# Performance work log

Measured on AMD Instinct MI355X. Metric: run time of the kernel, lower is better.

## Reference

```python
import jax, jax.numpy as jnp
import numpy as np

E = 1024
H = 16
DH = E // H
HID = E // 4  # sync_gate hidden


def setup_inputs() -> dict:
    key = jax.random.key(0)
    ks = jax.random.split(key, 16)
    s = lambda k, shp, fan_in: jax.random.normal(k, shp, dtype=jnp.float32) / np.sqrt(fan_in)
    return {
        "x": jax.random.normal(ks[0], (2, 2048, E), dtype=jnp.float32),
        "sync_features": jax.random.normal(ks[1], (2, E), dtype=jnp.float32),
        "Wq": s(ks[2], (E, E), E), "bq": jnp.zeros((E,), jnp.float32),
        "Wk": s(ks[3], (E, E), E), "bk": jnp.zeros((E,), jnp.float32),
        "Wv": s(ks[4], (E, E), E), "bv": jnp.zeros((E,), jnp.float32),
        "Ws1": s(ks[5], (E, HID), E), "bs1": jnp.zeros((HID,), jnp.float32),
        "Ws2": s(ks[6], (HID, H), HID), "bs2": jnp.zeros((H,), jnp.float32),
        "Wo": s(ks[7], (E, E), E), "bo": jnp.zeros((E,), jnp.float32),
    }


def reference(x, sync_features, Wq, bq, Wk, bk, Wv, bv, Ws1, bs1, Ws2, bs2, Wo, bo):
    B, S, _ = x.shape
    # QKV projections, split into heads: [B,S,H,DH]
    q = (x @ Wq + bq).reshape(B, S, H, DH)
    k = (x @ Wk + bk).reshape(B, S, H, DH)
    v = (x @ Wv + bv).reshape(B, S, H, DH)
    # scores: [B,H,S,S]
    scores = jnp.einsum('bihd,bjhd->bhij', q, k) / np.sqrt(DH).astype(np.float32)
    # per-head sync gate: [B,H] -> broadcast multiply BEFORE softmax
    sw = jax.nn.sigmoid(jax.nn.relu(sync_features @ Ws1 + bs1) @ Ws2 + bs2)
    scores = scores * sw[:, :, None, None]
    attn = jax.nn.softmax(scores, axis=-1)
    # dropout is identity in eval mode
    ctx = jnp.einsum('bhij,bjhd->bihd', attn, v).reshape(B, S, E)
    out = ctx @ Wo + bo
    return out, attn.mean(axis=1)
```

## Files before the change

### kernel.cpp

```cpp
#include <hip/hip_runtime.h>

#define B_ 2
#define S_ 2048
#define E_ 1024
#define H_ 16
#define DH_ 64
#define HID_ 256
#define M_ (B_*S_)

typedef __attribute__((ext_vector_type(8))) short s16x8;
typedef __attribute__((ext_vector_type(4))) float f32x4;
typedef unsigned int u32;
typedef unsigned short u16;
typedef u32 __attribute__((address_space(1))) gu32;
typedef u32 __attribute__((address_space(3))) lu32;

#define MFMA_B16(a,b,c) __builtin_amdgcn_mfma_f32_16x16x32_bf16((a),(b),(c),0,0,0)

__device__ __forceinline__ f32x4 fzero() { f32x4 z = {0.f, 0.f, 0.f, 0.f}; return z; }

__device__ __forceinline__ u16 f2bf(float x) {
    u32 u = __float_as_uint(x);
    u32 r = u + 0x7FFFu + ((u >> 16) & 1u);
    return (u16)(r >> 16);
}
__device__ __forceinline__ float bf2f(u16 b) {
    return __uint_as_float(((u32)b) << 16);
}
__device__ __forceinline__ void gload16(const void* gsrc, void* ldst) {
    __builtin_amdgcn_global_load_lds((const gu32*)gsrc, (lu32*)ldst, 16, 0, 0);
}
__device__ __forceinline__ s16x8 lds_frag(const u16* base, int byt) {
    return *(const s16x8*)((const char*)base + byt);
}

__global__ __launch_bounds__(256)
void zfill(float* __restrict__ out, int n)
{
    const int i = blockIdx.x * 256 + threadIdx.x;
    if (i < n) out[i] = 0.f;
}

__global__ __launch_bounds__(256)
void gate_kernel(const float* __restrict__ sync_f,
                 const float* __restrict__ Ws1, const float* __restrict__ bs1,
                 const float* __restrict__ Ws2, const float* __restrict__ bs2,
                 float* __restrict__ sw)
{
    __shared__ float xs[E_];
    __shared__ float hid[HID_];
    const int b = blockIdx.x, t = threadIdx.x;
    for (int i = t; i < E_; i += 256) xs[i] = sync_f[b * E_ + i];
    __syncthreads();
    float acc = bs1[t];
    for (int k = 0; k < E_; ++k) acc = fmaf(xs[k], Ws1[k * HID_ + t], acc);
    hid[t] = fmaxf(acc, 0.f);
    __syncthreads();
    if (t < H_) {
        float a = bs2[t];
        for (int k = 0; k < HID_; ++k) a = fmaf(hid[k], Ws2[k * H_ + t], a);
        sw[b * H_ + t] = 1.f / (1.f + __expf(-a));
    }
}

__global__ __launch_bounds__(256)
void split_x(const float* __restrict__ X, u16* __restrict__ Xhi, u16* __restrict__ Xlo)
{
    const int i = blockIdx.x * 256 + threadIdx.x;
    if (i >= M_ * E_ / 8) return;
    const float4 a = ((const float4*)X)[2 * i];
    const float4 bq = ((const float4*)X)[2 * i + 1];
    float v[8] = {a.x, a.y, a.z, a.w, bq.x, bq.y, bq.z, bq.w};
    s16x8 h, l;
#pragma unroll
    for (int e = 0; e < 8; ++e) {
        u16 hb = f2bf(v[e]);
        h[e] = (short)hb;
        l[e] = (short)f2bf(v[e] - bf2f(hb));
    }
    ((s16x8*)Xhi)[i] = h;
    ((s16x8*)Xlo)[i] = l;
}

__global__ __launch_bounds__(256)
void split_tw(const float* __restrict__ W, u16* __restrict__ Thi, u16* __restrict__ Tlo)
{
    __shared__ float t[64][65];
    const int k0 = blockIdx.y * 64;
    const int n0 = blockIdx.x * 64;
    const int tid = threadIdx.x;
    const int rr = tid >> 4;
    const int cc = (tid & 15) * 4;
#pragma unroll
    for (int p = 0; p < 4; ++p) {
        float4 v = *(const float4*)&W[(size_t)(k0 + p * 16 + rr) * E_ + n0 + cc];
        t[p * 16 + rr][cc + 0] = v.x;
        t[p * 16 + rr][cc + 1] = v.y;
        t[p * 16 + rr][cc + 2] = v.z;
        t[p * 16 + rr][cc + 3] = v.w;
    }
    __syncthreads();
    const int on = tid >> 2;
    const int ok = (tid & 3) * 16;
    s16x8 h0, h1, l0, l1;
#pragma unroll
    for (int j = 0; j < 8; ++j) {
        float v = t[ok + j][on];
        u16 hb = f2bf(v);
        h0[j] = (short)hb; l0[j] = (short)f2bf(v - bf2f(hb));
        float v2 = t[ok + 8 + j][on];
        u16 hb2 = f2bf(v2);
        h1[j] = (short)hb2; l1[j] = (short)f2bf(v2 - bf2f(hb2));
    }
    size_t o = (size_t)(n0 + on) * E_ + k0 + ok;
    *(s16x8*)&Thi[o] = h0;  *(s16x8*)&Thi[o + 8] = h1;
    *(s16x8*)&Tlo[o] = l0;  *(s16x8*)&Tlo[o + 8] = l1;
}

template<int MODE>
__global__ __launch_bounds__(256)
void gemm_mfma(const u16* __restrict__ Ahi, const u16* __restrict__ Alo,
               const u16* __restrict__ Bhi, const u16* __restrict__ Blo,
               const float* __restrict__ bias,
               float* __restrict__ OutF, u16* __restrict__ OutHi, u16* __restrict__ OutLo)
{
    __shared__ u16 lA[2][128 * 32];
    __shared__ u16 lB[2][128 * 32];
    const int m0 = blockIdx.y * 128, n0 = blockIdx.x * 128;
    const int tid = threadIdx.x;
    const int w = tid >> 6, l = tid & 63;
    const int l15 = l & 15, l4 = l >> 4;
    const int wm = w >> 1, wn = w & 1;

    f32x4 acc[4][4];
#pragma unroll
    for (int i = 0; i < 4; ++i)
#pragma unroll
        for (int j = 0; j < 4; ++j) acc[i][j] = fzero();

    for (int k0 = 0; k0 < E_; k0 += 32) {
        __syncthreads();
#pragma unroll
        for (int jj = 0; jj < 8; ++jj) {
            const int idx = w * 8 + jj, tt = idx >> 3, q = idx & 7;
            const int r = q * 16 + (l >> 2);
            const int s = l & 3;
            const int g = s ^ ((r >> 1) & 3);
            const u16* src;
            if (tt == 0)      src = Ahi + (size_t)(m0 + r) * E_ + k0 + 8 * g;
            else if (tt == 1) src = Alo + (size_t)(m0 + r) * E_ + k0 + 8 * g;
            else if (tt == 2) src = Bhi + (size_t)(n0 + r) * E_ + k0 + 8 * g;
            else              src = Blo + (size_t)(n0 + r) * E_ + k0 + 8 * g;
            u16* base = (tt < 2) ? lA[tt] : lB[tt - 2];
            gload16(src, (char*)base + q * 1024);
        }
        __syncthreads();

        s16x8 af[2][4];
#pragma unroll
        for (int hl = 0; hl < 2; ++hl)
#pragma unroll
            for (int mf = 0; mf < 4; ++mf) {
                const int row = wm * 64 + mf * 16 + l15;
                af[hl][mf] = lds_frag(lA[hl], row * 64 + ((l4 ^ ((row >> 1) & 3)) << 4));
            }
#pragma unroll
        for (int nf = 0; nf < 4; ++nf) {
            const int rowb = wn * 64 + nf * 16 + l15;
            const int byt = rowb * 64 + ((l4 ^ ((rowb >> 1) & 3)) << 4);
            s16x8 b0 = lds_frag(lB[0], byt);
            s16x8 b1 = lds_frag(lB[1], byt);
#pragma unroll
            for (int mf = 0; mf < 4; ++mf) {
                acc[mf][nf] = MFMA_B16(af[0][mf], b0, acc[mf][nf]);
                acc[mf][nf] = MFMA_B16(af[0][mf], b1, acc[mf][nf]);
                acc[mf][nf] = MFMA_B16(af[1][mf], b0, acc[mf][nf]);
            }
        }
    }

#pragma unroll
    for (int mf = 0; mf < 4; ++mf)
#pragma unroll
        for (int nf = 0; nf < 4; ++nf) {
            const int n = n0 + wn * 64 + nf * 16 + l15;
            const float bb = bias[n];
#pragma unroll
            for (int rr = 0; rr < 4; ++rr) {
                const int m = m0 + wm * 64 + mf * 16 + l4 * 4 + rr;
                const float v = acc[mf][nf][rr] + bb;
                if (MODE == 0) {
                    OutF[(size_t)m * E_ + n] = v;
                } else {
                    const int bat = m >> 11, s = m & (S_ - 1);
                    const int hh = n >> 6, dh = n & 63;
                    const size_t o = (MODE == 1)
                        ? (((size_t)(bat * H_ + hh) * S_ + s) * DH_ + dh)
                        : (((size_t)(bat * H_ + hh) * DH_ + dh) * S_ + s);
                    const u16 hb = f2bf(v);
                    OutHi[o] = hb;
                    OutLo[o] = f2bf(v - bf2f(hb));
                }
            }
        }
}

__global__ __launch_bounds__(256)
void attn_pass1(const u16* __restrict__ qhi, const u16* __restrict__ qlo,
                const u16* __restrict__ khi, const u16* __restrict__ klo,
                const u16* __restrict__ vthi, const u16* __restrict__ vtlo,
                const float* __restrict__ sw,
                u16* __restrict__ ctxhi, u16* __restrict__ ctxlo,
                float* __restrict__ invl)
{
    __shared__ u16 lK[2][64 * 64];
    __shared__ u16 lV[2][64 * 64];
    __shared__ float lP[128 * 64];
    const int b = blockIdx.z, h = blockIdx.y, i0 = blockIdx.x * 128;
    const int tid = threadIdx.x;
    const int w = tid >> 6, l = tid & 63;
    const int l15 = l & 15, l4 = l >> 4;
    const size_t bh = (size_t)(b * H_ + h);
    const float scl = sw[b * H_ + h] * 0.125f;

    s16x8 qf[2][2][2];
#pragma unroll
    for (int hl = 0; hl < 2; ++hl)
#pragma unroll
        for (int rf = 0; rf < 2; ++rf)
#pragma unroll
            for (int kc = 0; kc < 2; ++kc) {
                const int row = i0 + w * 32 + rf * 16 + l15;
                const u16* src = (hl ? qlo : qhi) + (bh * S_ + row) * DH_ + kc * 32 + 8 * l4;
                qf[hl][rf][kc] = *(const s16x8*)src;
            }

    f32x4 cacc[2][4];
    float l_acc[2][4];
#pragma unroll
    for (int rf = 0; rf < 2; ++rf) {
#pragma unroll
        for (int df = 0; df < 4; ++df) cacc[rf][df] = fzero();
#pragma unroll
        for (int rr = 0; rr < 4; ++rr) l_acc[rf][rr] = 0.f;
    }

    for (int j0 = 0; j0 < S_; j0 += 64) {
        __syncthreads();
#pragma unroll
        for (int jj = 0; jj < 8; ++jj) {
            const int idx = w * 8 + jj, tt = idx >> 3, q = idx & 7;
            const int r = q * 8 + (l >> 3);
            const int s = l & 7;
            const int g = s ^ (r & 7);
            const u16* src;
            if (tt == 0)      src = khi  + (bh * S_ + j0 + r) * DH_ + 8 * g;
            else if (tt == 1) src = klo  + (bh * S_ + j0 + r) * DH_ + 8 * g;
            else if (tt == 2) src = vthi + (bh * DH_ + r) * S_ + j0 + 8 * g;
            else              src = vtlo + (bh * DH_ + r) * S_ + j0 + 8 * g;
            u16* base = (tt < 2) ? lK[tt] : lV[tt - 2];
            gload16(src, (char*)base + q * 1024);
        }
        __syncthreads();

        f32x4 p[2][4];
#pragma unroll
        for (int rf = 0; rf < 2; ++rf)
#pragma unroll
            for (int nf = 0; nf < 4; ++nf) p[rf][nf] = fzero();
#pragma unroll
        for (int kc = 0; kc < 2; ++kc) {
            s16x8 kb[2][4];
#pragma unroll
            for (int hl = 0; hl < 2; ++hl)
#pragma unroll
                for (int nf = 0; nf < 4; ++nf) {
                    const int j = nf * 16 + l15;
                    kb[hl][nf] = lds_frag(lK[hl], j * 128 + (((kc * 4 + l4) ^ (j & 7)) << 4));
                }
#pragma unroll
            for (int rf = 0; rf < 2; ++rf)
#pragma unroll
                for (int nf = 0; nf < 4; ++nf) {
                    p[rf][nf] = MFMA_B16(qf[0][rf][kc], kb[0][nf], p[rf][nf]);
                    p[rf][nf] = MFMA_B16(qf[0][rf][kc], kb[1][nf], p[rf][nf]);
                    p[rf][nf] = MFMA_B16(qf[1][rf][kc], kb[0][nf], p[rf][nf]);
                }
        }
#pragma unroll
        for (int rf = 0; rf < 2; ++rf)
#pragma unroll
            for (int nf = 0; nf < 4; ++nf) {
                const int jcol = nf * 16 + l15;
#pragma unroll
                for (int rr = 0; rr < 4; ++rr) {
                    const float e = __expf(p[rf][nf][rr] * scl);
                    l_acc[rf][rr] += e;
                    const int irow = w * 32 + rf * 16 + l4 * 4 + rr;
                    const int byt = irow * 256 +
                        ((((jcol >> 2) ^ ((irow >> 1) & 7)) << 4) | ((jcol & 3) << 2));
                    *(float*)((char*)lP + byt) = e;
                }
            }
#pragma unroll
        for (int kc = 0; kc < 2; ++kc) {
            s16x8 vb[2][4];
#pragma unroll
            for (int hl = 0; hl < 2; ++hl)
#pragma unroll
                for (int df = 0; df < 4; ++df) {
                    const int d = df * 16 + l15;
                    vb[hl][df] = lds_frag(lV[hl], d * 128 + (((kc * 4 + l4) ^ (d & 7)) << 4));
                }
#pragma unroll
            for (int rf = 0; rf < 2; ++rf) {
                const int irow = w * 32 + rf * 16 + l15;
                const int msk = (irow >> 1) & 7;
                float pv8[8];
#pragma unroll
                for (int hh = 0; hh < 2; ++hh) {
                    const int slot = kc * 8 + 2 * l4 + hh;
                    const f32x4 t4 = *(const f32x4*)((const char*)lP +
                                        irow * 256 + ((slot ^ msk) << 4));
                    pv8[hh * 4 + 0] = t4[0]; pv8[hh * 4 + 1] = t4[1];
                    pv8[hh * 4 + 2] = t4[2]; pv8[hh * 4 + 3] = t4[3];
                }
                s16x8 ph, pl;
#pragma unroll
                for (int e = 0; e < 8; ++e) {
                    const u16 hb = f2bf(pv8[e]);
                    ph[e] = (short)hb;
                    pl[e] = (short)f2bf(pv8[e] - bf2f(hb));
                }
#pragma unroll
                for (int df = 0; df < 4; ++df) {
                    cacc[rf][df] = MFMA_B16(ph, vb[0][df], cacc[rf][df]);
                    cacc[rf][df] = MFMA_B16(ph, vb[1][df], cacc[rf][df]);
                    cacc[rf][df] = MFMA_B16(pl, vb[0][df], cacc[rf][df]);
                }
            }
        }
    }

#pragma unroll
    for (int rf = 0; rf < 2; ++rf)
#pragma unroll
        for (int rr = 0; rr < 4; ++rr) {
#pragma unroll
            for (int off = 1; off < 16; off <<= 1)
                l_acc[rf][rr] += __shfl_xor(l_acc[rf][rr], off);
        }
#pragma unroll
    for (int rf = 0; rf < 2; ++rf)
#pragma unroll
        for (int rr = 0; rr < 4; ++rr) {
            const float inv = 1.f / l_acc[rf][rr];
            const int srow = i0 + w * 32 + rf * 16 + l4 * 4 + rr;
            if (l15 == 0) invl[bh * S_ + srow] = inv;
#pragma unroll
            for (int df = 0; df < 4; ++df) {
                const float v = cacc[rf][df][rr] * inv;
                const size_t o = ((size_t)b * S_ + srow) * E_ + h * DH_ + df * 16 + l15;
                const u16 hb = f2bf(v);
                ctxhi[o] = hb;
                ctxlo[o] = f2bf(v - bf2f(hb));
            }
        }
}

__global__ __launch_bounds__(256)
void attn_mean(const u16* __restrict__ qhi, const u16* __restrict__ qlo,
               const u16* __restrict__ khi, const u16* __restrict__ klo,
               const float* __restrict__ sw, const float* __restrict__ invl,
               float* __restrict__ amean)
{
    __shared__ u16 lQ[2][128 * 64];
    __shared__ u16 lKm[2][128 * 64];
    const int b = blockIdx.z, i0 = blockIdx.y * 128, j0 = blockIdx.x * 128;
    const int tid = threadIdx.x;
    const int w = tid >> 6, l = tid & 63;
    const int l15 = l & 15, l4 = l >> 4;

    f32x4 acc[2][8];
#pragma unroll
    for (int rf = 0; rf < 2; ++rf)
#pragma unroll
        for (int nf = 0; nf < 8; ++nf) acc[rf][nf] = fzero();

    for (int h = 0; h < H_; ++h) {
        const size_t bh = (size_t)(b * H_ + h);
        __syncthreads();
#pragma unroll
        for (int jj = 0; jj < 16; ++jj) {
            const int idx = w * 16 + jj, tt = idx >> 4, q = idx & 15;
            const int r = q * 8 + (l >> 3);
            const int s = l & 7;
            const int g = s ^ (r & 7);
            const u16* bsrc = (tt == 0) ? qhi : (tt == 1) ? qlo : (tt == 2) ? khi : klo;
            const int row0 = (tt < 2) ? i0 : j0;
            const u16* src = bsrc + (bh * S_ + row0 + r) * DH_ + 8 * g;
            u16* base = (tt == 0) ? lQ[0] : (tt == 1) ? lQ[1]
                      : (tt == 2) ? lKm[0] : lKm[1];
            gload16(src, (char*)base + q * 1024);
        }
        __syncthreads();

        const float scl = sw[b * H_ + h] * 0.125f;
        float ivl[2][4];
#pragma unroll
        for (int rf = 0; rf < 2; ++rf)
#pragma unroll
            for (int rr = 0; rr < 4; ++rr)
                ivl[rf][rr] = invl[bh * S_ + i0 + w * 32 + rf * 16 + l4 * 4 + rr];

        f32x4 sc[2][8];
#pragma unroll
        for (int rf = 0; rf < 2; ++rf)
#pragma unroll
            for (int nf = 0; nf < 8; ++nf) sc[rf][nf] = fzero();
#pragma unroll
        for (int kc = 0; kc < 2; ++kc) {
            s16x8 qa[2][2];
#pragma unroll
            for (int hl = 0; hl < 2; ++hl)
#pragma unroll
                for (int rf = 0; rf < 2; ++rf) {
                    const int row = w * 32 + rf * 16 + l15;
                    qa[hl][rf] = lds_frag(lQ[hl],
                        row * 128 + (((kc * 4 + l4) ^ (row & 7)) << 4));
                }
#pragma unroll
            for (int nf = 0; nf < 8; ++nf) {
                const int j = nf * 16 + l15;
                const int byt = j * 128 + (((kc * 4 + l4) ^ (j & 7)) << 4);
                const s16x8 kb0 = lds_frag(lKm[0], byt);
                const s16x8 kb1 = lds_frag(lKm[1], byt);
#pragma unroll
                for (int rf = 0; rf < 2; ++rf) {
                    sc[rf][nf] = MFMA_B16(qa[0][rf], kb0, sc[rf][nf]);
                    sc[rf][nf] = MFMA_B16(qa[0][rf], kb1, sc[rf][nf]);
                    sc[rf][nf] = MFMA_B16(qa[1][rf], kb0, sc[rf][nf]);
                }
            }
        }
#pragma unroll
        for (int rf = 0; rf < 2; ++rf)
#pragma unroll
            for (int nf = 0; nf < 8; ++nf)
#pragma unroll
                for (int rr = 0; rr < 4; ++rr)
                    acc[rf][nf][rr] = fmaf(__expf(sc[rf][nf][rr] * scl), ivl[rf][rr],
                                           acc[rf][nf][rr]);
    }

#pragma unroll
    for (int rf = 0; rf < 2; ++rf)
#pragma unroll
        for (int nf = 0; nf < 8; ++nf)
#pragma unroll
            for (int rr = 0; rr < 4; ++rr) {
                const int row = i0 + w * 32 + rf * 16 + l4 * 4 + rr;
                amean[((size_t)b * S_ + row) * S_ + j0 + nf * 16 + l15] =
                    acc[rf][nf][rr] * (1.0f / H_);
            }
}

extern "C" void kernel_launch(void* const* d_in, const int* in_sizes, int n_in,
                              void* d_out, int out_size, void* d_ws, size_t ws_size,
                              hipStream_t stream) {
    (void)in_sizes; (void)n_in;
    const float* x     = (const float*)d_in[0];
    const float* syncf = (const float*)d_in[1];
    const float* Wq    = (const float*)d_in[2];
    const float* bq    = (const float*)d_in[3];
    const float* Wk    = (const float*)d_in[4];
    const float* bk    = (const float*)d_in[5];
    const float* Wv    = (const float*)d_in[6];
    const float* bv    = (const float*)d_in[7];
    const float* Ws1   = (const float*)d_in[8];
    const float* bs1   = (const float*)d_in[9];
    const float* Ws2   = (const float*)d_in[10];
    const float* bs2   = (const float*)d_in[11];
    const float* Wo    = (const float*)d_in[12];
    const float* bo    = (const float*)d_in[13];

    float* outp  = (float*)d_out;
    float* amean = outp + (size_t)M_ * E_;

    char* p = (char*)d_ws;
    auto alloc = [&](size_t bytes) {
        char* r = p; p += (bytes + 255) & ~(size_t)255; return r;
    };
    const size_t SZ_ME  = (size_t)M_ * E_ * 2;
    const size_t SZ_W   = (size_t)E_ * E_ * 2;
    float* swp  = (float*)alloc(128);
    u16* xhi    = (u16*)alloc(SZ_ME);
    u16* xlo    = (u16*)alloc(SZ_ME);
    u16* wt_hi  = (u16*)alloc(SZ_W);
    u16* wt_lo  = (u16*)alloc(SZ_W);
    u16* qh     = (u16*)alloc(SZ_ME);
    u16* ql     = (u16*)alloc(SZ_ME);
    u16* kh     = (u16*)alloc(SZ_ME);
    u16* kl     = (u16*)alloc(SZ_ME);
    u16* vth    = (u16*)alloc(SZ_ME);
    u16* vtl    = (u16*)alloc(SZ_ME);
    float* invl = (float*)alloc((size_t)B_ * H_ * S_ * 4);

    const size_t need = (size_t)(p - (char*)d_ws);
    if (ws_size < need) {
        const int n = out_size;
        zfill<<<dim3((n + 255) / 256), 256, 0, stream>>>(outp, n);
        return;
    }

    u16* ch = xhi;
    u16* cl = xlo;

    gate_kernel<<<dim3(B_), 256, 0, stream>>>(syncf, Ws1, bs1, Ws2, bs2, swp);
    split_x<<<dim3(M_ * E_ / 8 / 256), 256, 0, stream>>>(x, xhi, xlo);

    dim3 gt(16, 16);
    dim3 gg(E_ / 128, M_ / 128);
    split_tw<<<gt, 256, 0, stream>>>(Wq, wt_hi, wt_lo);
    gemm_mfma<1><<<gg, 256, 0, stream>>>(xhi, xlo, wt_hi, wt_lo, bq, nullptr, qh, ql);
    split_tw<<<gt, 256, 0, stream>>>(Wk, wt_hi, wt_lo);
    gemm_mfma<1><<<gg, 256, 0, stream>>>(xhi, xlo, wt_hi, wt_lo, bk, nullptr, kh, kl);
    split_tw<<<gt, 256, 0, stream>>>(Wv, wt_hi, wt_lo);
    gemm_mfma<2><<<gg, 256, 0, stream>>>(xhi, xlo, wt_hi, wt_lo, bv, nullptr, vth, vtl);

    attn_pass1<<<dim3(S_ / 128, H_, B_), 256, 0, stream>>>(qh, ql, kh, kl, vth, vtl,
                                                           swp, ch, cl, invl);

    attn_mean<<<dim3(S_ / 128, S_ / 128, B_), 256, 0, stream>>>(qh, ql, kh, kl,
                                                                swp, invl, amean);

    split_tw<<<gt, 256, 0, stream>>>(Wo, wt_hi, wt_lo);
    gemm_mfma<0><<<gg, 256, 0, stream>>>(ch, cl, wt_hi, wt_lo, bo, outp, nullptr, nullptr);
}
```

Measured before the change: 602.2 us.

## Double-buffer LDS tiles and widen GEMM/attention blocks to 512 threads

```diff
diff --git a/kernel.cpp b/kernel.cpp
--- a/kernel.cpp
+++ b/kernel.cpp
@@ -118,60 +118,64 @@
 }
 
 template<int MODE>
-__global__ __launch_bounds__(256)
+__global__ __launch_bounds__(512)
 void gemm_mfma(const u16* __restrict__ Ahi, const u16* __restrict__ Alo,
                const u16* __restrict__ Bhi, const u16* __restrict__ Blo,
                const float* __restrict__ bias,
                float* __restrict__ OutF, u16* __restrict__ OutHi, u16* __restrict__ OutLo)
 {
-    __shared__ u16 lA[2][128 * 32];
-    __shared__ u16 lB[2][128 * 32];
+    __shared__ u16 lA[2][2][128 * 32];
+    __shared__ u16 lB[2][2][128 * 32];
     const int m0 = blockIdx.y * 128, n0 = blockIdx.x * 128;
     const int tid = threadIdx.x;
     const int w = tid >> 6, l = tid & 63;
     const int l15 = l & 15, l4 = l >> 4;
     const int wm = w >> 1, wn = w & 1;
 
-    f32x4 acc[4][4];
-#pragma unroll
-    for (int i = 0; i < 4; ++i)
-#pragma unroll
-        for (int j = 0; j < 4; ++j) acc[i][j] = fzero();
-
-    for (int k0 = 0; k0 < E_; k0 += 32) {
-        __syncthreads();
-#pragma unroll
-        for (int jj = 0; jj < 8; ++jj) {
-            const int idx = w * 8 + jj, tt = idx >> 3, q = idx & 7;
+    auto stage = [&](int k0, int buf) {
+#pragma unroll
+        for (int jj = 0; jj < 4; ++jj) {
+            const int seg = w * 4 + jj, tt = seg >> 3, q = seg & 7;
             const int r = q * 16 + (l >> 2);
-            const int s = l & 3;
-            const int g = s ^ ((r >> 1) & 3);
+            const int g = (l & 3) ^ ((r >> 1) & 3);
             const u16* src;
             if (tt == 0)      src = Ahi + (size_t)(m0 + r) * E_ + k0 + 8 * g;
             else if (tt == 1) src = Alo + (size_t)(m0 + r) * E_ + k0 + 8 * g;
             else if (tt == 2) src = Bhi + (size_t)(n0 + r) * E_ + k0 + 8 * g;
             else              src = Blo + (size_t)(n0 + r) * E_ + k0 + 8 * g;
-            u16* base = (tt < 2) ? lA[tt] : lB[tt - 2];
+            u16* base = (tt < 2) ? lA[buf][tt] : lB[buf][tt - 2];
             gload16(src, (char*)base + q * 1024);
         }
+    };
+
+    f32x4 acc[2][4];
+#pragma unroll
+    for (int i = 0; i < 2; ++i)
+#pragma unroll
+        for (int j = 0; j < 4; ++j) acc[i][j] = fzero();
+
+    stage(0, 0);
+    for (int ks = 0; ks < 32; ++ks) {
+        const int buf = ks & 1;
         __syncthreads();
-
-        s16x8 af[2][4];
+        if (ks + 1 < 32) stage((ks + 1) * 32, buf ^ 1);
+
+        s16x8 af[2][2];
 #pragma unroll
         for (int hl = 0; hl < 2; ++hl)
 #pragma unroll
-            for (int mf = 0; mf < 4; ++mf) {
-                const int row = wm * 64 + mf * 16 + l15;
-                af[hl][mf] = lds_frag(lA[hl], row * 64 + ((l4 ^ ((row >> 1) & 3)) << 4));
+            for (int mf = 0; mf < 2; ++mf) {
+                const int row = wm * 32 + mf * 16 + l15;
+                af[hl][mf] = lds_frag(lA[buf][hl], row * 64 + ((l4 ^ ((row >> 1) & 3)) << 4));
             }
 #pragma unroll
         for (int nf = 0; nf < 4; ++nf) {
             const int rowb = wn * 64 + nf * 16 + l15;
             const int byt = rowb * 64 + ((l4 ^ ((rowb >> 1) & 3)) << 4);
-            s16x8 b0 = lds_frag(lB[0], byt);
-            s16x8 b1 = lds_frag(lB[1], byt);
-#pragma unroll
-            for (int mf = 0; mf < 4; ++mf) {
+            s16x8 b0 = lds_frag(lB[buf][0], byt);
+            s16x8 b1 = lds_frag(lB[buf][1], byt);
+#pragma unroll
+            for (int mf = 0; mf < 2; ++mf) {
                 acc[mf][nf] = MFMA_B16(af[0][mf], b0, acc[mf][nf]);
                 acc[mf][nf] = MFMA_B16(af[0][mf], b1, acc[mf][nf]);
                 acc[mf][nf] = MFMA_B16(af[1][mf], b0, acc[mf][nf]);
@@ -180,14 +184,14 @@
     }
 
 #pragma unroll
-    for (int mf = 0; mf < 4; ++mf)
+    for (int mf = 0; mf < 2; ++mf)
 #pragma unroll
         for (int nf = 0; nf < 4; ++nf) {
             const int n = n0 + wn * 64 + nf * 16 + l15;
             const float bb = bias[n];
 #pragma unroll
             for (int rr = 0; rr < 4; ++rr) {
-                const int m = m0 + wm * 64 + mf * 16 + l4 * 4 + rr;
+                const int m = m0 + wm * 32 + mf * 16 + l4 * 4 + rr;
                 const float v = acc[mf][nf][rr] + bb;
                 if (MODE == 0) {
                     OutF[(size_t)m * E_ + n] = v;
@@ -205,7 +209,7 @@
         }
 }
 
-__global__ __launch_bounds__(256)
+__global__ __launch_bounds__(512)
 void attn_pass1(const u16* __restrict__ qhi, const u16* __restrict__ qlo,
                 const u16* __restrict__ khi, const u16* __restrict__ klo,
                 const u16* __restrict__ vthi, const u16* __restrict__ vtlo,
@@ -213,55 +217,59 @@
                 u16* __restrict__ ctxhi, u16* __restrict__ ctxlo,
                 float* __restrict__ invl)
 {
-    __shared__ u16 lK[2][64 * 64];
-    __shared__ u16 lV[2][64 * 64];
-    __shared__ float lP[128 * 64];
-    const int b = blockIdx.z, h = blockIdx.y, i0 = blockIdx.x * 128;
+    __shared__ u16 lK[2][2][64 * 64];
+    __shared__ u16 lV[2][2][64 * 64];
+    __shared__ float lP[256 * 64];
+    const int b = blockIdx.z, h = blockIdx.y, i0 = blockIdx.x * 256;
     const int tid = threadIdx.x;
     const int w = tid >> 6, l = tid & 63;
     const int l15 = l & 15, l4 = l >> 4;
     const size_t bh = (size_t)(b * H_ + h);
     const float scl = sw[b * H_ + h] * 0.125f;
 
-    s16x8 qf[2][2][2];
-#pragma unroll
-    for (int hl = 0; hl < 2; ++hl)
-#pragma unroll
-        for (int rf = 0; rf < 2; ++rf)
-#pragma unroll
-            for (int kc = 0; kc < 2; ++kc) {
-                const int row = i0 + w * 32 + rf * 16 + l15;
-                const u16* src = (hl ? qlo : qhi) + (bh * S_ + row) * DH_ + kc * 32 + 8 * l4;
-                qf[hl][rf][kc] = *(const s16x8*)src;
-            }
-
-    f32x4 cacc[2][4];
-    float l_acc[2][4];
-#pragma unroll
-    for (int rf = 0; rf < 2; ++rf) {
-#pragma unroll
-        for (int df = 0; df < 4; ++df) cacc[rf][df] = fzero();
-#pragma unroll
-        for (int rr = 0; rr < 4; ++rr) l_acc[rf][rr] = 0.f;
-    }
-
-    for (int j0 = 0; j0 < S_; j0 += 64) {
-        __syncthreads();
-#pragma unroll
-        for (int jj = 0; jj < 8; ++jj) {
-            const int idx = w * 8 + jj, tt = idx >> 3, q = idx & 7;
+    auto stage_kv = [&](int j0, int buf) {
+#pragma unroll
+        for (int jj = 0; jj < 4; ++jj) {
+            const int seg = w * 4 + jj, tt = seg >> 3, q = seg & 7;
             const int r = q * 8 + (l >> 3);
-            const int s = l & 7;
-            const int g = s ^ (r & 7);
+            const int g = (l & 7) ^ (r & 7);
             const u16* src;
             if (tt == 0)      src = khi  + (bh * S_ + j0 + r) * DH_ + 8 * g;
             else if (tt == 1) src = klo  + (bh * S_ + j0 + r) * DH_ + 8 * g;
             else if (tt == 2) src = vthi + (bh * DH_ + r) * S_ + j0 + 8 * g;
             else              src = vtlo + (bh * DH_ + r) * S_ + j0 + 8 * g;
-            u16* base = (tt < 2) ? lK[tt] : lV[tt - 2];
+            u16* base = (tt < 2) ? lK[buf][tt] : lV[buf][tt - 2];
             gload16(src, (char*)base + q * 1024);
         }
+    };
+
+    s16x8 qf[2][2][2];
+#pragma unroll
+    for (int hl = 0; hl < 2; ++hl)
+#pragma unroll
+        for (int rf = 0; rf < 2; ++rf)
+#pragma unroll
+            for (int kc = 0; kc < 2; ++kc) {
+                const int row = i0 + w * 32 + rf * 16 + l15;
+                const u16* src = (hl ? qlo : qhi) + (bh * S_ + row) * DH_ + kc * 32 + 8 * l4;
+                qf[hl][rf][kc] = *(const s16x8*)src;
+            }
+
+    f32x4 cacc[2][4];
+    float l_acc[2][4];
+#pragma unroll
+    for (int rf = 0; rf < 2; ++rf) {
+#pragma unroll
+        for (int df = 0; df < 4; ++df) cacc[rf][df] = fzero();
+#pragma unroll
+        for (int rr = 0; rr < 4; ++rr) l_acc[rf][rr] = 0.f;
+    }
+
+    stage_kv(0, 0);
+    for (int jt = 0; jt < S_ / 64; ++jt) {
+        const int buf = jt & 1;
         __syncthreads();
+        if (jt + 1 < S_ / 64) stage_kv((jt + 1) * 64, buf ^ 1);
 
         f32x4 p[2][4];
 #pragma unroll
@@ -276,7 +284,8 @@
 #pragma unroll
                 for (int nf = 0; nf < 4; ++nf) {
                     const int j = nf * 16 + l15;
-                    kb[hl][nf] = lds_frag(lK[hl], j * 128 + (((kc * 4 + l4) ^ (j & 7)) << 4));
+                    kb[hl][nf] = lds_frag(lK[buf][hl],
+                        j * 128 + (((kc * 4 + l4) ^ (j & 7)) << 4));
                 }
 #pragma unroll
             for (int rf = 0; rf < 2; ++rf)
@@ -310,7 +319,8 @@
 #pragma unroll
                 for (int df = 0; df < 4; ++df) {
                     const int d = df * 16 + l15;
-                    vb[hl][df] = lds_frag(lV[hl], d * 128 + (((kc * 4 + l4) ^ (d & 7)) << 4));
+                    vb[hl][df] = lds_frag(lV[buf][hl],
+                        d * 128 + (((kc * 4 + l4) ^ (d & 7)) << 4));
                 }
 #pragma unroll
             for (int rf = 0; rf < 2; ++rf) {
@@ -374,38 +384,51 @@
                const float* __restrict__ sw, const float* __restrict__ invl,
                float* __restrict__ amean)
 {
-    __shared__ u16 lQ[2][128 * 64];
-    __shared__ u16 lKm[2][128 * 64];
+    __shared__ u16 lKm[2][2][128 * 64];
     const int b = blockIdx.z, i0 = blockIdx.y * 128, j0 = blockIdx.x * 128;
     const int tid = threadIdx.x;
     const int w = tid >> 6, l = tid & 63;
     const int l15 = l & 15, l4 = l >> 4;
 
+    auto stage_k = [&](int h, int buf) {
+        const size_t bh = (size_t)(b * H_ + h);
+#pragma unroll
+        for (int jj = 0; jj < 8; ++jj) {
+            const int seg = w * 8 + jj, tt = seg >> 4, q = seg & 15;
+            const int r = q * 8 + (l >> 3);
+            const int g = (l & 7) ^ (r & 7);
+            const u16* src = (tt ? klo : khi) + (bh * S_ + j0 + r) * DH_ + 8 * g;
+            gload16(src, (char*)lKm[buf][tt] + q * 1024);
+        }
+    };
+
     f32x4 acc[2][8];
 #pragma unroll
     for (int rf = 0; rf < 2; ++rf)
 #pragma unroll
         for (int nf = 0; nf < 8; ++nf) acc[rf][nf] = fzero();
 
+    stage_k(0, 0);
     for (int h = 0; h < H_; ++h) {
+        const int buf = h & 1;
+        __syncthreads();
+        if (h + 1 < H_) stage_k(h + 1, buf ^ 1);
+
         const size_t bh = (size_t)(b * H_ + h);
-        __syncthreads();
-#pragma unroll
-        for (int jj = 0; jj < 16; ++jj) {
-            const int idx = w * 16 + jj, tt = idx >> 4, q = idx & 15;
-            const int r = q * 8 + (l >> 3);
-            const int s = l & 7;
-            const int g = s ^ (r & 7);
-            const u16* bsrc = (tt == 0) ? qhi : (tt == 1) ? qlo : (tt == 2) ? khi : klo;
-            const int row0 = (tt < 2) ? i0 : j0;
-            const u16* src = bsrc + (bh * S_ + row0 + r) * DH_ + 8 * g;
-            u16* base = (tt == 0) ? lQ[0] : (tt == 1) ? lQ[1]
-                      : (tt == 2) ? lKm[0] : lKm[1];
-            gload16(src, (char*)base + q * 1024);
-        }
-        __syncthreads();
-
         const float scl = sw[b * H_ + h] * 0.125f;
+
+        s16x8 qa[2][2][2];
+#pragma unroll
+        for (int hl = 0; hl < 2; ++hl)
+#pragma unroll
+            for (int rf = 0; rf < 2; ++rf)
+#pragma unroll
+                for (int kc = 0; kc < 2; ++kc) {
+                    const int row = i0 + w * 32 + rf * 16 + l15;
+                    const u16* src = (hl ? qlo : qhi) + (bh * S_ + row) * DH_
+                                     + kc * 32 + 8 * l4;
+                    qa[hl][rf][kc] = *(const s16x8*)src;
+                }
         float ivl[2][4];
 #pragma unroll
         for (int rf = 0; rf < 2; ++rf)
@@ -420,26 +443,17 @@
             for (int nf = 0; nf < 8; ++nf) sc[rf][nf] = fzero();
 #pragma unroll
         for (int kc = 0; kc < 2; ++kc) {
-            s16x8 qa[2][2];
-#pragma unroll
-            for (int hl = 0; hl < 2; ++hl)
-#pragma unroll
-                for (int rf = 0; rf < 2; ++rf) {
-                    const int row = w * 32 + rf * 16 + l15;
-                    qa[hl][rf] = lds_frag(lQ[hl],
-                        row * 128 + (((kc * 4 + l4) ^ (row & 7)) << 4));
-                }
 #pragma unroll
             for (int nf = 0; nf < 8; ++nf) {
                 const int j = nf * 16 + l15;
                 const int byt = j * 128 + (((kc * 4 + l4) ^ (j & 7)) << 4);
-                const s16x8 kb0 = lds_frag(lKm[0], byt);
-                const s16x8 kb1 = lds_frag(lKm[1], byt);
+                const s16x8 kb0 = lds_frag(lKm[buf][0], byt);
+                const s16x8 kb1 = lds_frag(lKm[buf][1], byt);
 #pragma unroll
                 for (int rf = 0; rf < 2; ++rf) {
-                    sc[rf][nf] = MFMA_B16(qa[0][rf], kb0, sc[rf][nf]);
-                    sc[rf][nf] = MFMA_B16(qa[0][rf], kb1, sc[rf][nf]);
-                    sc[rf][nf] = MFMA_B16(qa[1][rf], kb0, sc[rf][nf]);
+                    sc[rf][nf] = MFMA_B16(qa[0][rf][kc], kb0, sc[rf][nf]);
+                    sc[rf][nf] = MFMA_B16(qa[0][rf][kc], kb1, sc[rf][nf]);
+                    sc[rf][nf] = MFMA_B16(qa[1][rf][kc], kb0, sc[rf][nf]);
                 }
             }
         }
@@ -508,8 +522,7 @@
 
     const size_t need = (size_t)(p - (char*)d_ws);
     if (ws_size < need) {
-        const int n = out_size;
-        zfill<<<dim3((n + 255) / 256), 256, 0, stream>>>(outp, n);
+        zfill<<<dim3((out_size + 255) / 256), 256, 0, stream>>>(outp, out_size);
         return;
     }
 
@@ -522,18 +535,18 @@
     dim3 gt(16, 16);
     dim3 gg(E_ / 128, M_ / 128);
     split_tw<<<gt, 256, 0, stream>>>(Wq, wt_hi, wt_lo);
-    gemm_mfma<1><<<gg, 256, 0, stream>>>(xhi, xlo, wt_hi, wt_lo, bq, nullptr, qh, ql);
+    gemm_mfma<1><<<gg, 512, 0, stream>>>(xhi, xlo, wt_hi, wt_lo, bq, nullptr, qh, ql);
     split_tw<<<gt, 256, 0, stream>>>(Wk, wt_hi, wt_lo);
-    gemm_mfma<1><<<gg, 256, 0, stream>>>(xhi, xlo, wt_hi, wt_lo, bk, nullptr, kh, kl);
+    gemm_mfma<1><<<gg, 512, 0, stream>>>(xhi, xlo, wt_hi, wt_lo, bk, nullptr, kh, kl);
     split_tw<<<gt, 256, 0, stream>>>(Wv, wt_hi, wt_lo);
-    gemm_mfma<2><<<gg, 256, 0, stream>>>(xhi, xlo, wt_hi, wt_lo, bv, nullptr, vth, vtl);
-
-    attn_pass1<<<dim3(S_ / 128, H_, B_), 256, 0, stream>>>(qh, ql, kh, kl, vth, vtl,
+    gemm_mfma<2><<<gg, 512, 0, stream>>>(xhi, xlo, wt_hi, wt_lo, bv, nullptr, vth, vtl);
+
+    attn_pass1<<<dim3(S_ / 256, H_, B_), 512, 0, stream>>>(qh, ql, kh, kl, vth, vtl,
                                                            swp, ch, cl, invl);
 
     attn_mean<<<dim3(S_ / 128, S_ / 128, B_), 256, 0, stream>>>(qh, ql, kh, kl,
                                                                 swp, invl, amean);
 
     split_tw<<<gt, 256, 0, stream>>>(Wo, wt_hi, wt_lo);
-    gemm_mfma<0><<<gg, 256, 0, stream>>>(ch, cl, wt_hi, wt_lo, bo, outp, nullptr, nullptr);
-}
+    gemm_mfma<0><<<gg, 512, 0, stream>>>(ch, cl, wt_hi, wt_lo, bo, outp, nullptr, nullptr);
+}
```

New measurement: 510.2 us. -15.3%, faster.
